# Kernel tuning notes

Hardware: AMD Instinct MI355X
Metric: run time of the kernel (lower is better)

The kernel has to match this reference:

```python
import jax, jax.numpy as jnp
import numpy as np


def setup_inputs() -> dict:
    key = jax.random.key(0)
    ks = jax.random.split(key, 7)
    B, Hde, E, Hf, Wf, Catt = 256, 512, 512, 8, 32, 512
    return {
        "h": jax.random.normal(ks[0], (B, Hde), dtype=jnp.float32),
        "x_em": jax.random.normal(ks[1], (B, E, Hf, Wf), dtype=jnp.float32),
        "att_x_em": jax.random.normal(ks[2], (B, Hf * Wf, Catt), dtype=jnp.float32),
        "Wh": jax.random.normal(ks[3], (E, Hde), dtype=jnp.float32) * (1.0 / np.sqrt(Hde)),
        "bh": jax.random.normal(ks[4], (E,), dtype=jnp.float32) * 0.02,
        "Wa": jax.random.normal(ks[5], (E,), dtype=jnp.float32) * (1.0 / np.sqrt(E)),
        "ba": jax.random.normal(ks[6], (), dtype=jnp.float32) * 0.02,
        "feature_h": Hf,
        "feature_w": Wf,
    }


def reference(h, x_em, att_x_em, Wh, bh, Wa, ba, feature_h, feature_w):
    # h: [B, Hde]; 1x1 conv on [B,Hde,1,1] == linear layer
    B = h.shape[0]
    g_em = h @ Wh.T + bh                                   # [B, E]
    # broadcast-add g_em over spatial, tanh (dropout = identity in eval)
    feat = jnp.tanh(x_em + g_em[:, :, None, None])         # [B, E, H, W]
    # conv_att: 1x1 conv E -> 1 == weighted channel sum
    scores = jnp.einsum('behw,e->bhw', feat, Wa) + ba      # [B, H, W]
    alpha = jax.nn.softmax(scores.reshape(B, feature_h * feature_w), axis=-1)  # [B, HW]
    att_out = jnp.einsum('bs,bsc->bc', alpha, att_x_em)    # [B, Catt]
    return att_out, alpha.reshape(B, 1, feature_h * feature_w)
```

## Files before the change

kernel.cpp:

```cpp
#include <hip/hip_runtime.h>

#define BB 256
#define E 512
#define HDE 512
#define HW 256
#define CATT 512
#define NT 1024
#define NW (NT / 64)

__device__ __forceinline__ float fast_tanh(float x) {
    float e = __expf(2.0f * x);
    float r = __builtin_amdgcn_rcpf(1.0f + e);
    return 1.0f - 2.0f * r;
}

__global__ __launch_bounds__(NT, 4) void fused_attn(
        const float* __restrict__ h, const float* __restrict__ x_em,
        const float* __restrict__ att, const float* __restrict__ Wh,
        const float* __restrict__ bh, const float* __restrict__ Wa,
        float* __restrict__ out) {
    const int b = blockIdx.x;
    const int t = threadIdx.x;
    const int lane = t & 63;
    const int w = t >> 6;

    __shared__ float sH[HDE];
    __shared__ float sG[E];
    __shared__ float sWa[E];
    __shared__ float sAlpha[HW];
    __shared__ float sred[8];
    __shared__ float4 sBuf4[NW * 64];
    float* sBuf = (float*)sBuf4;

    if (t < HDE / 4)
        ((float4*)sH)[t] = ((const float4*)(h + (size_t)b * HDE))[t];
    __syncthreads();

    {
        const int e = t >> 1;
        const int half = t & 1;
        const float* wrow = Wh + (size_t)e * HDE + half * (HDE / 2);
        const float* hrow = sH + half * (HDE / 2);
        float acc = 0.0f;
#pragma unroll 8
        for (int i = 0; i < HDE / 8; ++i) {
            float4 wv = ((const float4*)wrow)[i];
            float4 hv = ((const float4*)hrow)[i];
            acc += wv.x * hv.x + wv.y * hv.y + wv.z * hv.z + wv.w * hv.w;
        }
        acc += __shfl_xor(acc, 1);
        if (half == 0) {
            sG[e] = acc + bh[e];
            sWa[e] = Wa[e];
        }
    }
    __syncthreads();

    {
        const float* xb = x_em + ((size_t)b * E + (size_t)w * (E / NW)) * HW + lane * 4;
        float4 acc = {0.f, 0.f, 0.f, 0.f};
#pragma unroll 8
        for (int i = 0; i < E / NW; ++i) {
            float4 x = *(const float4*)(xb + (size_t)i * HW);
            const int e = w * (E / NW) + i;
            const float g = sG[e];
            const float wa = sWa[e];
            acc.x += wa * fast_tanh(x.x + g);
            acc.y += wa * fast_tanh(x.y + g);
            acc.z += wa * fast_tanh(x.z + g);
            acc.w += wa * fast_tanh(x.w + g);
        }
        sBuf4[w * 64 + lane] = acc;
    }
    __syncthreads();

    float v = 0.f, p = 0.f;
    if (t < HW) {
        #pragma unroll
        for (int g = 0; g < NW; ++g) v += sBuf[g * HW + t];
        float m = v;
        #pragma unroll
        for (int o = 32; o; o >>= 1) m = fmaxf(m, __shfl_xor(m, o));
        if (lane == 0) sred[w] = m;
    }
    __syncthreads();
    if (t < HW) {
        float m = fmaxf(fmaxf(sred[0], sred[1]), fmaxf(sred[2], sred[3]));
        p = __expf(v - m);
        float s = p;
        #pragma unroll
        for (int o = 32; o; o >>= 1) s += __shfl_xor(s, o);
        if (lane == 0) sred[4 + w] = s;
    }
    __syncthreads();
    if (t < HW) {
        float s = sred[4] + sred[5] + sred[6] + sred[7];
        float a = p / s;
        sAlpha[t] = a;
        out[(size_t)BB * CATT + (size_t)b * HW + t] = a;
    }
    __syncthreads();

    {
        const int c4 = t & 127;
        const int g = t >> 7;
        const float* ab = att + ((size_t)b * HW + g) * CATT + c4 * 4;
        float4 acc = {0.f, 0.f, 0.f, 0.f};
#pragma unroll 8
        for (int i = 0; i < HW / 8; ++i) {
            float4 x = *(const float4*)(ab + (size_t)i * 8 * CATT);
            const float a = sAlpha[g + i * 8];
            acc.x += a * x.x;
            acc.y += a * x.y;
            acc.z += a * x.z;
            acc.w += a * x.w;
        }
        sBuf4[g * 128 + c4] = acc;
    }
    __syncthreads();

    if (t < CATT / 4) {
        float4 acc = sBuf4[t];
        #pragma unroll
        for (int g = 1; g < 8; ++g) {
            float4 x = sBuf4[g * 128 + t];
            acc.x += x.x; acc.y += x.y; acc.z += x.z; acc.w += x.w;
        }
        ((float4*)(out + (size_t)b * CATT))[t] = acc;
    }
}

extern "C" void kernel_launch(void* const* d_in, const int* in_sizes, int n_in,
                              void* d_out, int out_size, void* d_ws, size_t ws_size,
                              hipStream_t stream) {
    const float* h    = (const float*)d_in[0];
    const float* x_em = (const float*)d_in[1];
    const float* att  = (const float*)d_in[2];
    const float* Wh   = (const float*)d_in[3];
    const float* bh   = (const float*)d_in[4];
    const float* Wa   = (const float*)d_in[5];

    float* out = (float*)d_out;

    fused_attn<<<dim3(BB), NT, 0, stream>>>(h, x_em, att, Wh, bh, Wa, out);
}
```

Before: 318.6 us.

## Split fused attention into two kernels with a four-way split over channels

Replaces the single 1024-thread-per-batch fused kernel with two 256-thread kernels launched on a (B, 4) grid. The first computes the channel-sliced projection and partial scores and writes them to workspace. The second sums the partials, recomputes the softmax redundantly in each of the four blocks, and does a channel-sliced weighted sum over att_x_em. The aim is more, smaller blocks so the 256-block grid fills more of the GPU. The cost is an extra launch, a workspace round-trip, and the softmax repeated four times per batch.

```diff
diff --git a/kernel.cpp b/kernel.cpp
--- a/kernel.cpp
+++ b/kernel.cpp
@@ -5,8 +5,9 @@
 #define HDE 512
 #define HW 256
 #define CATT 512
-#define NT 1024
-#define NW (NT / 64)
+#define Q 4
+#define ECH (E / Q)
+#define CCH (CATT / Q)
 
 __device__ __forceinline__ float fast_tanh(float x) {
     float e = __expf(2.0f * x);
@@ -14,119 +15,126 @@
     return 1.0f - 2.0f * r;
 }
 
-__global__ __launch_bounds__(NT, 4) void fused_attn(
+__global__ __launch_bounds__(256, 8) void k_scores(
         const float* __restrict__ h, const float* __restrict__ x_em,
-        const float* __restrict__ att, const float* __restrict__ Wh,
-        const float* __restrict__ bh, const float* __restrict__ Wa,
-        float* __restrict__ out) {
-    const int b = blockIdx.x;
-    const int t = threadIdx.x;
-    const int lane = t & 63;
-    const int w = t >> 6;
+        const float* __restrict__ Wh, const float* __restrict__ bh,
+        const float* __restrict__ Wa, float* __restrict__ scoresPart) {
+    const int b = blockIdx.x, q = blockIdx.y;
+    const int t = threadIdx.x, lane = t & 63, w = t >> 6;
 
-    __shared__ float sH[HDE];
-    __shared__ float sG[E];
-    __shared__ float sWa[E];
-    __shared__ float sAlpha[HW];
-    __shared__ float sred[8];
-    __shared__ float4 sBuf4[NW * 64];
-    float* sBuf = (float*)sBuf4;
+    __shared__ float sG[ECH];
+    __shared__ float sWa[ECH];
+    __shared__ float4 sPart[4][HW / 4];
 
-    if (t < HDE / 4)
-        ((float4*)sH)[t] = ((const float4*)(h + (size_t)b * HDE))[t];
-    __syncthreads();
+    const float* hp = h + (size_t)b * HDE + lane * 8;
+    const float4 h0 = *(const float4*)hp;
+    const float4 h1 = *(const float4*)(hp + 4);
 
-    {
-        const int e = t >> 1;
-        const int half = t & 1;
-        const float* wrow = Wh + (size_t)e * HDE + half * (HDE / 2);
-        const float* hrow = sH + half * (HDE / 2);
-        float acc = 0.0f;
-#pragma unroll 8
-        for (int i = 0; i < HDE / 8; ++i) {
-            float4 wv = ((const float4*)wrow)[i];
-            float4 hv = ((const float4*)hrow)[i];
-            acc += wv.x * hv.x + wv.y * hv.y + wv.z * hv.z + wv.w * hv.w;
-        }
-        acc += __shfl_xor(acc, 1);
-        if (half == 0) {
-            sG[e] = acc + bh[e];
-            sWa[e] = Wa[e];
+#pragma unroll 4
+    for (int i = 0; i < 32; ++i) {
+        const int el = w * 32 + i;
+        const int e = q * ECH + el;
+        const float* wr = Wh + (size_t)e * HDE + lane * 8;
+        float4 w0 = *(const float4*)wr;
+        float4 w1 = *(const float4*)(wr + 4);
+        float acc = w0.x * h0.x + w0.y * h0.y + w0.z * h0.z + w0.w * h0.w
+                  + w1.x * h1.x + w1.y * h1.y + w1.z * h1.z + w1.w * h1.w;
+#pragma unroll
+        for (int o = 32; o; o >>= 1) acc += __shfl_xor(acc, o);
+        if (lane == 0) {
+            sG[el] = acc + bh[e];
+            sWa[el] = Wa[e];
         }
     }
     __syncthreads();
 
     {
-        const float* xb = x_em + ((size_t)b * E + (size_t)w * (E / NW)) * HW + lane * 4;
+        const float* xb = x_em + ((size_t)b * E + (size_t)q * ECH + (size_t)w * 32) * HW
+                        + (size_t)lane * 4;
         float4 acc = {0.f, 0.f, 0.f, 0.f};
 #pragma unroll 8
-        for (int i = 0; i < E / NW; ++i) {
+        for (int i = 0; i < 32; ++i) {
             float4 x = *(const float4*)(xb + (size_t)i * HW);
-            const int e = w * (E / NW) + i;
-            const float g = sG[e];
-            const float wa = sWa[e];
+            const float g = sG[w * 32 + i];
+            const float wa = sWa[w * 32 + i];
             acc.x += wa * fast_tanh(x.x + g);
             acc.y += wa * fast_tanh(x.y + g);
             acc.z += wa * fast_tanh(x.z + g);
             acc.w += wa * fast_tanh(x.w + g);
         }
-        sBuf4[w * 64 + lane] = acc;
+        sPart[w][lane] = acc;
     }
     __syncthreads();
 
-    float v = 0.f, p = 0.f;
-    if (t < HW) {
-        #pragma unroll
-        for (int g = 0; g < NW; ++g) v += sBuf[g * HW + t];
-        float m = v;
-        #pragma unroll
-        for (int o = 32; o; o >>= 1) m = fmaxf(m, __shfl_xor(m, o));
-        if (lane == 0) sred[w] = m;
+    if (t < HW / 4) {
+        float4 a0 = sPart[0][t], a1 = sPart[1][t], a2 = sPart[2][t], a3 = sPart[3][t];
+        float4 r;
+        r.x = a0.x + a1.x + a2.x + a3.x;
+        r.y = a0.y + a1.y + a2.y + a3.y;
+        r.z = a0.z + a1.z + a2.z + a3.z;
+        r.w = a0.w + a1.w + a2.w + a3.w;
+        *(float4*)(scoresPart + ((size_t)q * BB + b) * HW + t * 4) = r;
     }
+}
+
+__global__ __launch_bounds__(256, 8) void k_att(
+        const float* __restrict__ scoresPart, const float* __restrict__ att,
+        float* __restrict__ out) {
+    const int b = blockIdx.x, q = blockIdx.y;
+    const int t = threadIdx.x, lane = t & 63, w = t >> 6;
+
+    __shared__ float sAlpha[HW];
+    __shared__ float sred[8];
+    __shared__ float4 sPar[8][CCH / 4];
+
+    float v = 0.f;
+#pragma unroll
+    for (int p = 0; p < Q; ++p)
+        v += scoresPart[((size_t)p * BB + b) * HW + t];
+
+    float m = v;
+#pragma unroll
+    for (int o = 32; o; o >>= 1) m = fmaxf(m, __shfl_xor(m, o));
+    if (lane == 0) sred[w] = m;
     __syncthreads();
-    if (t < HW) {
-        float m = fmaxf(fmaxf(sred[0], sred[1]), fmaxf(sred[2], sred[3]));
-        p = __expf(v - m);
-        float s = p;
-        #pragma unroll
-        for (int o = 32; o; o >>= 1) s += __shfl_xor(s, o);
-        if (lane == 0) sred[4 + w] = s;
-    }
+    m = fmaxf(fmaxf(sred[0], sred[1]), fmaxf(sred[2], sred[3]));
+    float p = __expf(v - m);
+    float s = p;
+#pragma unroll
+    for (int o = 32; o; o >>= 1) s += __shfl_xor(s, o);
+    if (lane == 0) sred[4 + w] = s;
     __syncthreads();
-    if (t < HW) {
-        float s = sred[4] + sred[5] + sred[6] + sred[7];
-        float a = p / s;
-        sAlpha[t] = a;
-        out[(size_t)BB * CATT + (size_t)b * HW + t] = a;
+    s = sred[4] + sred[5] + sred[6] + sred[7];
+    const float a = p / s;
+    sAlpha[t] = a;
+    if (q == 0) out[(size_t)BB * CATT + (size_t)b * HW + t] = a;
+    __syncthreads();
+
+    {
+        const int c4 = t & 31, sg = t >> 5;
+        const float* ab = att + ((size_t)b * HW + sg) * CATT + (size_t)q * CCH + c4 * 4;
+        float4 acc = {0.f, 0.f, 0.f, 0.f};
+#pragma unroll 8
+        for (int i = 0; i < 32; ++i) {
+            float4 x = *(const float4*)(ab + (size_t)(8 * i) * CATT);
+            const float al = sAlpha[sg + 8 * i];
+            acc.x += al * x.x;
+            acc.y += al * x.y;
+            acc.z += al * x.z;
+            acc.w += al * x.w;
+        }
+        sPar[sg][c4] = acc;
     }
     __syncthreads();
 
-    {
-        const int c4 = t & 127;
-        const int g = t >> 7;
-        const float* ab = att + ((size_t)b * HW + g) * CATT + c4 * 4;
-        float4 acc = {0.f, 0.f, 0.f, 0.f};
-#pragma unroll 8
-        for (int i = 0; i < HW / 8; ++i) {
-            float4 x = *(const float4*)(ab + (size_t)i * 8 * CATT);
-            const float a = sAlpha[g + i * 8];
-            acc.x += a * x.x;
-            acc.y += a * x.y;
-            acc.z += a * x.z;
-            acc.w += a * x.w;
+    if (t < CCH / 4) {
+        float4 r = sPar[0][t];
+#pragma unroll
+        for (int g = 1; g < 8; ++g) {
+            float4 x = sPar[g][t];
+            r.x += x.x; r.y += x.y; r.z += x.z; r.w += x.w;
         }
-        sBuf4[g * 128 + c4] = acc;
-    }
-    __syncthreads();
-
-    if (t < CATT / 4) {
-        float4 acc = sBuf4[t];
-        #pragma unroll
-        for (int g = 1; g < 8; ++g) {
-            float4 x = sBuf4[g * 128 + t];
-            acc.x += x.x; acc.y += x.y; acc.z += x.z; acc.w += x.w;
-        }
-        ((float4*)(out + (size_t)b * CATT))[t] = acc;
+        *(float4*)(out + (size_t)b * CATT + (size_t)q * CCH + t * 4) = r;
     }
 }
 
@@ -141,6 +149,8 @@
     const float* Wa   = (const float*)d_in[5];
 
     float* out = (float*)d_out;
+    float* scoresPart = (float*)d_ws;
 
-    fused_attn<<<dim3(BB), NT, 0, stream>>>(h, x_em, att, Wh, bh, Wa, out);
+    k_scores<<<dim3(BB, Q), 256, 0, stream>>>(h, x_em, Wh, bh, Wa, scoresPart);
+    k_att<<<dim3(BB, Q), 256, 0, stream>>>(scoresPart, att, out);
 }
```

Result: no change. 315.7 us (-0.9%).
